# Kernel optimization log

Hardware: AMD Instinct MI355X
Metric: run time of the kernel (lower is better)

## Reference

```python
import jax, jax.numpy as jnp
import numpy as np

B, N, C, D, K, H, A = 4, 2048, 128, 128, 16, 64, 512


def _rn(k, shape, s):
    return (jax.random.normal(k, shape) * s).astype(jnp.float32)


def setup_inputs():
    ks = jax.random.split(jax.random.key(0), 40)
    w = lambda i, o, c: _rn(ks[i], (o, c), 0.02)
    b = lambda i, o: _rn(ks[i + 20], (o,), 0.02)
    p = {}
    p["xyz"] = _rn(ks[0], (B, 3, N), 1.0)
    p["pos"] = _rn(ks[1], (B, 2, N), 1.0)
    p["key"] = _rn(ks[2], (B, C, N), 1.0)
    p["query"] = _rn(ks[3], (B, C, N), 1.0)
    p["mv_w1"] = w(4, C, 2 * C); p["mv_b1"] = b(4, C)
    p["mv_w2"] = w(5, C, C);     p["mv_b2"] = b(5, C)
    p["mv_ws"] = w(6, C, 2 * C); p["mv_bs"] = b(6, C)
    p["wk"] = w(7, D, C); p["bk"] = b(7, D)
    p["wq"] = w(8, D, C); p["bq"] = b(8, D)
    p["wv"] = w(9, D, C); p["bv"] = b(9, D)
    p["xyz_w1"] = w(10, H, 3); p["xyz_b1"] = b(10, H)
    p["xyz_w2"] = w(11, D, H); p["xyz_b2"] = b(11, D)
    p["pos_w1"] = w(12, H, 2); p["pos_b1"] = b(12, H)
    p["pos_w2"] = w(13, D, H); p["pos_b2"] = b(13, D)
    p["xat_w1"] = w(14, A, D); p["xat_b1"] = b(14, A)
    p["xat_w2"] = w(15, D, A); p["xat_b2"] = b(15, D)
    p["at_w1"] = w(16, A, D); p["at_b1"] = b(16, A)
    p["at_w2"] = w(17, D, A); p["at_b2"] = b(17, D)
    p["wkq"] = w(18, C, D); p["bkq"] = b(18, C)
    p["wend"] = w(19, C, D); p["bend"] = b(19, C)
    return p


def c1(w, b, x):  # 1x1 Conv1d: (O,C) on (B,C,N)
    return jnp.einsum('oc,bcn->bon', w, x) + b[None, :, None]


def c2(w, b, x):  # 1x1 Conv2d: (O,C) on (B,C,N,K)
    return jnp.einsum('oc,bcnk->bonk', w, x) + b[None, :, None, None]


def mlp2(w1, b1, w2, b2, x):
    return c2(w2, b2, jax.nn.relu(c2(w1, b1, x)))


def softmax_one(x):  # exp(x-m) / (1 + sum exp(x-m)) over last axis
    m = jnp.max(x, axis=-1, keepdims=True)
    e = jnp.exp(x - m)
    return e / (1.0 + jnp.sum(e, axis=-1, keepdims=True))


def knn_idx(pts, k):  # pts: (B, N, d) -> (B, N, k) indices, include_self=True
    sq = jnp.sum(pts * pts, axis=-1)
    d2 = sq[:, :, None] + sq[:, None, :] - 2.0 * jnp.einsum('bnd,bmd->bnm', pts, pts)
    return jnp.argsort(d2, axis=-1)[:, :, :k]


def group(f, idx):  # f: (B,C,N), idx: (B,N,K) -> (B,C,N,K)
    return jax.vmap(lambda a, i: a[:, i])(f, idx)


def reference(xyz, pos, key, query, mv_w1, mv_b1, mv_w2, mv_b2, mv_ws, mv_bs,
              wk, bk, wq, bq, wv, bv, xyz_w1, xyz_b1, xyz_w2, xyz_b2,
              pos_w1, pos_b1, pos_w2, pos_b2, xat_w1, xat_b1, xat_w2, xat_b2,
              at_w1, at_b1, at_w2, at_b2, wkq, bkq, wend, bend):
    cat = jnp.concatenate([key, query], axis=1)  # (B, 2C, N)
    # MLP_Res
    value = c1(mv_w2, mv_b2, jax.nn.relu(c1(mv_w1, mv_b1, cat))) + c1(mv_ws, mv_bs, cat)
    identity = value
    k = c1(wk, bk, key)
    q = c1(wq, bq, query)
    v = c1(wv, bv, value)
    # ---- block 1: xyz-space kNN attention ----
    idx1 = knn_idx(jnp.swapaxes(xyz, 1, 2), K)           # (B,N,K)
    kq_rel = k[..., None] - group(q, idx1)               # (B,D,N,K)
    xyz_rel = xyz[..., None] - group(xyz, idx1)          # (B,3,N,K)
    xyz_emb = mlp2(xyz_w1, xyz_b1, xyz_w2, xyz_b2, xyz_rel)
    xa = softmax_one(mlp2(xat_w1, xat_b1, xat_w2, xat_b2, kq_rel + xyz_emb))
    agg = jnp.sum(xa * (v[..., None] + xyz_emb), axis=-1)  # (B,D,N)
    value = c1(wkq, bkq, agg) + identity
    value = c1(wv, bv, value)
    # ---- block 2: pos-space kNN attention ----
    idx2 = knn_idx(jnp.swapaxes(pos, 1, 2), K)
    qk_rel = q[..., None] - group(k, idx2)
    pos_rel = pos[..., None] - group(pos, idx2)
    pos_emb = mlp2(pos_w1, pos_b1, pos_w2, pos_b2, pos_rel)
    at = softmax_one(mlp2(at_w1, at_b1, at_w2, at_b2, qk_rel + pos_emb))
    agg = jnp.sum(at * (value[..., None] + pos_emb), axis=-1)
    y = c1(wend, bend, agg)
    return y + identity
```

## Files before the change

kernel.cpp:

```cpp
#include <hip/hip_runtime.h>
#include <hip/hip_bf16.h>

typedef __hip_bfloat16 bf16;
typedef unsigned long long ull;

#define BB 4
#define NN 2048
#define CCH 128
#define DDM 128
#define KNB 16
#define HHD 64
#define AAD 512
#define PP (BB*NN)

typedef __attribute__((ext_vector_type(8))) short short8;
typedef __attribute__((ext_vector_type(16))) float f32x16;

__device__ __forceinline__ float b2f(bf16 x) { return __bfloat162float(x); }
__device__ __forceinline__ bf16 f2b(float x) { return __float2bfloat16(x); }

__device__ __forceinline__ float ldany(const void* p, size_t i, int f32) {
  return f32 ? ((const float*)p)[i] : __bfloat162float(((const bf16*)p)[i]);
}

__device__ __forceinline__ long pack4(float a, float b, float c, float d) {
  union { bf16 h[4]; long l; } u;
  u.h[0] = f2b(a); u.h[1] = f2b(b); u.h[2] = f2b(c); u.h[3] = f2b(d);
  return u.l;
}
__device__ __forceinline__ void unpack4(long l, float* o) {
  union { bf16 h[4]; long l; } u; u.l = l;
  o[0] = b2f(u.h[0]); o[1] = b2f(u.h[1]); o[2] = b2f(u.h[2]); o[3] = b2f(u.h[3]);
}

__device__ __forceinline__ short8 ldfrag(const bf16* base, int row, int stride, int k0, int hl) {
  const bf16* p = base + (size_t)row * stride + k0 + (hl << 3);
  union { short8 v; long l[2]; } u;
  u.l[0] = *(const long*)p;
  u.l[1] = *(const long*)(p + 4);
  return u.v;
}

__device__ __forceinline__ f32x16 MFMA(short8 a, short8 b, f32x16 c) {
  return __builtin_amdgcn_mfma_f32_32x32x16_bf16(a, b, c, 0, 0, 0);
}

struct PtrArr { const void* p[36]; int n[36]; };
struct CvtTab { int src[16]; int off[16]; int n[16]; int isb[16]; };
struct G4 { const bf16* X[4]; int K[4]; int woff[4]; int boff[4]; bf16* out[4]; int relu[4]; };

__global__ __launch_bounds__(256) void sniff_kern(PtrArr pa, int* __restrict__ flags) {
  int t = blockIdx.x;
  const bf16* x = (const bf16*)pa.p[t];
  int n = pa.n[t]; if (n > 4096) n = 4096;
  __shared__ int cnt;
  if (threadIdx.x == 0) cnt = 0;
  __syncthreads();
  int c = 0;
  for (int i = threadIdx.x; i < n; i += 256) {
    float v = fabsf(__bfloat162float(x[i]));
    if (v == 0.f || (v >= 1e-6f && v <= 1024.f)) c++;
  }
  atomicAdd(&cnt, c);
  __syncthreads();
  if (threadIdx.x == 0) flags[t] = (cnt >= (n * 7) / 8) ? 0 : 1;
}

__global__ __launch_bounds__(256) void cvtprep_kern(PtrArr pa, CvtTab tab,
                                                    const int* __restrict__ flags,
                                                    bf16* __restrict__ warena, float* __restrict__ barena,
                                                    bf16* __restrict__ w1img0, bf16* __restrict__ w2img0,
                                                    bf16* __restrict__ cw2img0, float* __restrict__ fb0,
                                                    bf16* __restrict__ w1img1, bf16* __restrict__ w2img1,
                                                    bf16* __restrict__ cw2img1, float* __restrict__ fb1) {
  int y = blockIdx.y;
  if (y >= 2) {
    int e = y - 2;
    int i = blockIdx.x * 256 + threadIdx.x;
    if (i >= tab.n[e]) return;
    float v = ldany(pa.p[tab.src[e]], i, flags[tab.src[e]]);
    if (tab.isb[e]) barena[tab.off[e] + i] = v;
    else warena[tab.off[e] + i] = f2b(v);
    return;
  }
  int set = y;
  int cIdx = set ? 20 : 16, aIdx = set ? 28 : 24, dd = set ? 2 : 3;
  bf16* w1img = set ? w1img1 : w1img0;
  bf16* w2img = set ? w2img1 : w2img0;
  bf16* cw2img = set ? cw2img1 : cw2img0;
  float* fb = set ? fb1 : fb0;
  const void* cw1 = pa.p[cIdx];     const void* cb1 = pa.p[cIdx + 1];
  const void* cw2 = pa.p[cIdx + 2]; const void* cb2 = pa.p[cIdx + 3];
  const void* aw1 = pa.p[aIdx];     const void* ab1 = pa.p[aIdx + 1];
  const void* aw2 = pa.p[aIdx + 2]; const void* ab2 = pa.p[aIdx + 3];
  int i = blockIdx.x * 256 + threadIdx.x;
  const int fcw1 = flags[cIdx], fcb1 = flags[cIdx + 1];
  const int fcw2 = flags[cIdx + 2], fcb2 = flags[cIdx + 3];
  const int faw1 = flags[aIdx], fab1 = flags[aIdx + 1];
  const int faw2 = flags[aIdx + 2], fab2 = flags[aIdx + 3];
  float* ab1f = fb;
  float* ab2f = fb + 512;
  float* cb1f = fb + 640;
  float* cb2f = fb + 704;
  float* cw1f = fb + 832;
  if (i < 65536) {
    int hg = i >> 7, c = i & 127;
    w1img[(size_t)hg * 132 + c] = f2b(ldany(aw1, i, faw1));
  } else if (i < 131072) {
    int j = i - 65536;
    int o = j >> 9, hh = j & 511;
    int ac = hh >> 7, hloc = hh & 127;
    w2img[(size_t)(ac * 128 + o) * 132 + hloc] = f2b(ldany(aw2, j, faw2));
  } else if (i < 139264) {
    int j = i - 131072;
    int o = j >> 6, h = j & 63;
    cw2img[o * 68 + h] = f2b(ldany(cw2, j, fcw2));
  } else if (i < 139776) {
    int j = i - 139264; ab1f[j] = ldany(ab1, j, fab1);
  } else if (i < 139904) {
    int j = i - 139776; ab2f[j] = ldany(ab2, j, fab2);
  } else if (i < 139968) {
    int j = i - 139904; cb1f[j] = ldany(cb1, j, fcb1);
  } else if (i < 140096) {
    int j = i - 139968; cb2f[j] = ldany(cb2, j, fcb2);
  } else if (i < 140288) {
    int j = i - 140096;
    int h = j / 3, c = j % 3;
    cw1f[j] = (c < dd) ? ldany(cw1, h * dd + c, fcw1) : 0.f;
  }
}

__global__ __launch_bounds__(256) void trall_kern(const void* __restrict__ keyp,
                                                  const void* __restrict__ qryp,
                                                  const void* __restrict__ xyzp,
                                                  const void* __restrict__ posp,
                                                  const int* __restrict__ flags,
                                                  bf16* __restrict__ catT,
                                                  float* __restrict__ xyzT,
                                                  float* __restrict__ posT) {
  int bx = blockIdx.x;
  if (bx < 512) {
    __shared__ float tile[64][65];
    int xx = bx & 31, yy = (bx >> 5) & 1, zz = bx >> 6;
    int b = zz & 3, half = zz >> 2;
    const void* src = half ? qryp : keyp;
    const int f32 = flags[2 + half];
    int n0 = xx * 64, c0 = yy * 64;
    int tx = threadIdx.x & 63, ty = threadIdx.x >> 6;
    for (int r = ty; r < 64; r += 4)
      tile[r][tx] = ldany(src, (size_t)(b * 128 + c0 + r) * NN + n0 + tx, f32);
    __syncthreads();
    for (int r = ty; r < 64; r += 4)
      catT[(size_t)(b * NN + n0 + r) * 256 + half * 128 + c0 + tx] = __float2bfloat16(tile[tx][r]);
    return;
  }
  int cb = bx - 512;
  int which = cb >> 7;
  const void* src = which ? posp : xyzp;
  float* dst = which ? posT : xyzT;
  int dd = which ? 2 : 3;
  const int f32 = flags[which];
  int i = (cb & 127) * 256 * 2 + threadIdx.x;
  for (int rep = 0; rep < 2; ++rep, i += 256) {
    if (i < PP * 4) {
      int p = i >> 2, j = i & 3;
      int b = p >> 11, n = p & (NN - 1);
      dst[i] = (j < dd) ? ldany(src, (size_t)(b * dd + j) * NN + n, f32) : 0.f;
    }
  }
}

__global__ __launch_bounds__(512) void mega_kern(
    const float* __restrict__ xyzT, const float* __restrict__ posT,
    int* __restrict__ idx1, int* __restrict__ idx2,
    G4 g, const bf16* __restrict__ warena, const float* __restrict__ barena) {
  __shared__ __attribute__((aligned(16))) char smem[33280];
  int bx = blockIdx.x;
  int tid = threadIdx.x, lane = tid & 63, wvv = tid >> 6;
  if (bx < 2048) {
    float4* cds = (float4*)smem;
    int set = bx >> 10;
    int pblk = bx & 1023;
    const float* coordsT = set ? posT : xyzT;
    int* idxout = set ? idx2 : idx1;
    int p0 = pblk * 8, b = p0 >> 11;
    for (int j = tid; j < NN; j += 512)
      cds[j] = *(const float4*)&coordsT[((size_t)(b << 11) + j) * 4];
    __syncthreads();
    int p = p0 + wvv, n = p & (NN - 1);
    float4 cc = cds[n];
    float sqi = __fadd_rn(__fadd_rn(__fmul_rn(cc.x, cc.x), __fmul_rn(cc.y, cc.y)),
                          __fmul_rn(cc.z, cc.z));
    ull t[32];
#pragma unroll
    for (int s = 0; s < 32; ++s) {
      int j = (s << 6) | lane;
      float4 q = cds[j];
      float sqj = __fadd_rn(__fadd_rn(__fmul_rn(q.x, q.x), __fmul_rn(q.y, q.y)),
                            __fmul_rn(q.z, q.z));
      float dt  = __fadd_rn(__fadd_rn(__fmul_rn(cc.x, q.x), __fmul_rn(cc.y, q.y)),
                            __fmul_rn(cc.z, q.z));
      float d2 = __fsub_rn(__fadd_rn(sqi, sqj), __fmul_rn(2.f, dt));
      unsigned u = __float_as_uint(d2);
      u = (u & 0x80000000u) ? ~u : (u | 0x80000000u);
      t[s] = ((ull)u << 32) | (unsigned)j;
    }
#pragma unroll
    for (int k = 2; k <= 32; k <<= 1) {
#pragma unroll
      for (int j = k >> 1; j > 0; j >>= 1) {
#pragma unroll
        for (int i = 0; i < 32; ++i) {
          int l = i ^ j;
          if (l > i) {
            bool up = ((i & k) == 0);
            ull a = t[i], c = t[l];
            ull lo = a < c ? a : c;
            ull hi = a < c ? c : a;
            t[i] = up ? lo : hi;
            t[l] = up ? hi : lo;
          }
        }
      }
    }
    for (int r = 0; r < KNB; ++r) {
      ull h = t[0];
      ull m = h;
#pragma unroll
      for (int off = 1; off < 64; off <<= 1) {
        ull o = __shfl_xor(m, off);
        m = o < m ? o : m;
      }
      if (lane == 0) idxout[(size_t)p * KNB + r] = (int)(m & 0xffffffffu);
      if (h == m) {
#pragma unroll
        for (int i = 0; i < 15; ++i) t[i] = t[i + 1];
        t[15] = ~0ull;
      }
    }
    return;
  }
  {
    bf16* XT = (bf16*)smem;
    int bx2 = bx - 2048;
    int op = bx2 >> 7, ptile = bx2 & 127;
    const bf16* X = g.X[op];
    int K = g.K[op];
    const bf16* Wb = warena + g.woff[op];
    const float* bias = barena + g.boff[op];
    bf16* out = g.out[op];
    int relu = g.relu[op];
    int hl = lane >> 5, cA = lane & 31;
    int p0 = ptile * 64;
    int SK = K + 4;
    int kc = K >> 3;
    for (int c = tid; c < 64 * kc; c += 512) {
      int r = c / kc, col = (c % kc) << 3;
      *(float4*)&XT[r * SK + col] = *(const float4*)&X[(size_t)(p0 + r) * 256 + col];
    }
    __syncthreads();
    int o0 = (wvv & 3) * 32;
    int tt = wvv >> 2;
    f32x16 acc;
#pragma unroll
    for (int r = 0; r < 16; ++r) {
      int o = o0 + (r & 3) + 8 * (r >> 2) + 4 * hl;
      acc[r] = bias[o];
    }
    for (int ks = 0; ks < (K >> 4); ++ks) {
      short8 af = ldfrag(Wb, o0 + cA, K, ks * 16, hl);
      short8 b0 = ldfrag(XT, tt * 32 + cA, SK, ks * 16, hl);
      acc = MFMA(af, b0, acc);
    }
    int m = p0 + tt * 32 + cA;
#pragma unroll
    for (int q = 0; q < 4; ++q) {
      int ob = o0 + 8 * q + 4 * hl;
      float v[4] = {acc[4*q+0], acc[4*q+1], acc[4*q+2], acc[4*q+3]};
      if (relu) {
        v[0] = fmaxf(v[0], 0.f); v[1] = fmaxf(v[1], 0.f);
        v[2] = fmaxf(v[2], 0.f); v[3] = fmaxf(v[3], 0.f);
      }
      *(long*)(out + (size_t)m * 128 + ob) = pack4(v[0], v[1], v[2], v[3]);
    }
  }
}

__global__ __launch_bounds__(256) void gemm_chain_kern(
    const bf16* __restrict__ X, const bf16* __restrict__ warena,
    const float* __restrict__ barena,
    int w1off, int b1off, const bf16* __restrict__ add1, bf16* __restrict__ out1,
    int w2off, int b2off, bf16* __restrict__ out2) {
  __shared__ __attribute__((aligned(16))) bf16 XT[32 * 132];
  __shared__ __attribute__((aligned(16))) bf16 YT[32 * 132];
  int tid = threadIdx.x, lane = tid & 63, wv = tid >> 6;
  int hl = lane >> 5, cA = lane & 31;
  int p0 = blockIdx.x * 32;
  for (int c = tid; c < 32 * 16; c += 256) {
    int r = c >> 4, col = (c & 15) << 3;
    *(float4*)&XT[r * 132 + col] = *(const float4*)&X[(size_t)(p0 + r) * 128 + col];
  }
  __syncthreads();
  int o0 = wv * 32;
  const bf16* W1 = warena + w1off;
  const float* b1 = barena + b1off;
  f32x16 acc;
#pragma unroll
  for (int r = 0; r < 16; ++r) {
    int o = o0 + (r & 3) + 8 * (r >> 2) + 4 * hl;
    acc[r] = b1[o];
  }
#pragma unroll
  for (int ks = 0; ks < 8; ++ks) {
    short8 af = ldfrag(W1, o0 + cA, 128, ks * 16, hl);
    short8 b0 = ldfrag(XT, cA, 132, ks * 16, hl);
    acc = MFMA(af, b0, acc);
  }
  int m = p0 + cA;
#pragma unroll
  for (int q = 0; q < 4; ++q) {
    int ob = o0 + 8 * q + 4 * hl;
    float v[4] = {acc[4*q+0], acc[4*q+1], acc[4*q+2], acc[4*q+3]};
    if (add1) {
      float av[4];
      unpack4(*(const long*)(add1 + (size_t)m * 128 + ob), av);
      v[0] += av[0]; v[1] += av[1]; v[2] += av[2]; v[3] += av[3];
    }
    long pk = pack4(v[0], v[1], v[2], v[3]);
    *(long*)&YT[cA * 132 + ob] = pk;
    if (out1) *(long*)(out1 + (size_t)m * 128 + ob) = pk;
  }
  __syncthreads();
  const bf16* W2 = warena + w2off;
  const float* b2 = barena + b2off;
  f32x16 acc2;
#pragma unroll
  for (int r = 0; r < 16; ++r) {
    int o = o0 + (r & 3) + 8 * (r >> 2) + 4 * hl;
    acc2[r] = b2[o];
  }
#pragma unroll
  for (int ks = 0; ks < 8; ++ks) {
    short8 af = ldfrag(W2, o0 + cA, 128, ks * 16, hl);
    short8 b0 = ldfrag(YT, cA, 132, ks * 16, hl);
    acc2 = MFMA(af, b0, acc2);
  }
#pragma unroll
  for (int q = 0; q < 4; ++q) {
    int ob = o0 + 8 * q + 4 * hl;
    *(long*)(out2 + (size_t)m * 128 + ob) =
        pack4(acc2[4*q+0], acc2[4*q+1], acc2[4*q+2], acc2[4*q+3]);
  }
}

__global__ __launch_bounds__(256) void gemm32_kern(
    const bf16* __restrict__ X,
    const bf16* __restrict__ Wb, const float* __restrict__ bias,
    const bf16* __restrict__ add, bf16* __restrict__ out, int relu,
    void* __restrict__ outT, const int* __restrict__ flags) {
  __shared__ __attribute__((aligned(16))) bf16 XT[32 * 132];
  int tid = threadIdx.x, lane = tid & 63, wv = tid >> 6;
  int hl = lane >> 5, cA = lane & 31;
  int p0 = blockIdx.x * 32;
  for (int c = tid; c < 32 * 16; c += 256) {
    int r = c >> 4, col = (c & 15) << 3;
    *(float4*)&XT[r * 132 + col] = *(const float4*)&X[(size_t)(p0 + r) * 128 + col];
  }
  __syncthreads();
  int o0 = wv * 32;
  f32x16 acc;
#pragma unroll
  for (int r = 0; r < 16; ++r) {
    int o = o0 + (r & 3) + 8 * (r >> 2) + 4 * hl;
    acc[r] = bias[o];
  }
#pragma unroll
  for (int ks = 0; ks < 8; ++ks) {
    short8 af = ldfrag(Wb, o0 + cA, 128, ks * 16, hl);
    short8 b0 = ldfrag(XT, cA, 132, ks * 16, hl);
    acc = MFMA(af, b0, acc);
  }
  int m = p0 + cA;
  int f32o = outT ? flags[2] : 0;
  int b = m >> 11, n = m & (NN - 1);
#pragma unroll
  for (int q = 0; q < 4; ++q) {
    int ob = o0 + 8 * q + 4 * hl;
    float v[4] = {acc[4*q+0], acc[4*q+1], acc[4*q+2], acc[4*q+3]};
    if (add) {
      float av[4];
      unpack4(*(const long*)(add + (size_t)m * 128 + ob), av);
      v[0] += av[0]; v[1] += av[1]; v[2] += av[2]; v[3] += av[3];
    }
    if (relu) {
      v[0] = fmaxf(v[0], 0.f); v[1] = fmaxf(v[1], 0.f);
      v[2] = fmaxf(v[2], 0.f); v[3] = fmaxf(v[3], 0.f);
    }
    if (outT) {
#pragma unroll
      for (int i = 0; i < 4; ++i) {
        size_t oi = (size_t)(b * 128 + ob + i) * NN + n;
        if (f32o) ((float*)outT)[oi] = v[i];
        else ((bf16*)outT)[oi] = f2b(v[i]);
      }
    } else {
      *(long*)(out + (size_t)m * 128 + ob) = pack4(v[0], v[1], v[2], v[3]);
    }
  }
}

#define SMEM_BYTES 72192
__global__ __launch_bounds__(512, 4) void attn_mfma(
    const bf16* __restrict__ centerT, const bf16* __restrict__ gatherT,
    const float* __restrict__ coordsT, const bf16* __restrict__ vfeatT,
    const int* __restrict__ idx,
    const bf16* __restrict__ w1img, const bf16* __restrict__ w2img,
    const bf16* __restrict__ cw2img, const float* __restrict__ fb,
    bf16* __restrict__ aggT) {
  extern __shared__ char smem[];
  bf16* XS  = (bf16*)(smem);
  bf16* HT  = (bf16*)(smem + 33792);
  bf16* HC  = HT;
  bf16* CFE = (bf16*)(smem + 67584);
  bf16* VF  = (bf16*)(smem + 69632);
  int*  NID = (int*)(smem + 71680);
  const float* ab1f = fb;
  const float* ab2f = fb + 512;
  const float* cb1f = fb + 640;
  const float* cb2f = fb + 704;
  const float* cw1f = fb + 832;

  int tid = threadIdx.x, lane = tid & 63, wv = tid >> 6;
  int hl = lane >> 5, cA = lane & 31;
  int P0 = blockIdx.x * 8, b = P0 >> 11;

  if (tid < 128) NID[tid] = (b << 11) + idx[(size_t)(P0 + (tid >> 4)) * KNB + (tid & 15)];
  for (int i = tid; i < 1024; i += 512) {
    int g = i >> 7, d = i & 127;
    CFE[i] = centerT[(size_t)(P0 + g) * 128 + d];
    VF[i]  = vfeatT[(size_t)(P0 + g) * 128 + d];
  }
  __syncthreads();

  {
    int m = tid >> 2, sub = tid & 3;
    float4 ccd = *(const float4*)&coordsT[(size_t)(P0 + (m >> 4)) * 4];
    float4 nbd = *(const float4*)&coordsT[(size_t)NID[m] * 4];
    float r0 = ccd.x - nbd.x, r1 = ccd.y - nbd.y, r2 = ccd.z - nbd.z;
    int h0 = sub * 16;
    for (int hh = h0; hh < h0 + 16; hh += 4) {
      float a0 = fmaxf(cb1f[hh+0] + cw1f[(hh+0)*3]*r0 + cw1f[(hh+0)*3+1]*r1 + cw1f[(hh+0)*3+2]*r2, 0.f);
      float a1 = fmaxf(cb1f[hh+1] + cw1f[(hh+1)*3]*r0 + cw1f[(hh+1)*3+1]*r1 + cw1f[(hh+1)*3+2]*r2, 0.f);
      float a2 = fmaxf(cb1f[hh+2] + cw1f[(hh+2)*3]*r0 + cw1f[(hh+2)*3+1]*r1 + cw1f[(hh+2)*3+2]*r2, 0.f);
      float a3 = fmaxf(cb1f[hh+3] + cw1f[(hh+3)*3]*r0 + cw1f[(hh+3)*3+1]*r1 + cw1f[(hh+3)*3+2]*r2, 0.f);
      *(long*)&HC[m * 68 + hh] = pack4(a0, a1, a2, a3);
    }
    const bf16* grow = gatherT + (size_t)NID[m] * 128 + sub * 32;
    const bf16* crow = CFE + ((m >> 4) << 7) + sub * 32;
    for (int j = 0; j < 32; j += 4) {
      float gv[4], cv[4];
      unpack4(*(const long*)(grow + j), gv);
      unpack4(*(const long*)(crow + j), cv);
      *(long*)&XS[m * 132 + sub * 32 + j] =
          pack4(cv[0] - gv[0], cv[1] - gv[1], cv[2] - gv[2], cv[3] - gv[3]);
    }
  }
  __syncthreads();

  int r0s = (wv & 3) * 32;
  int mt0 = (wv >> 2) * 64;

  short8 pf[8];
#pragma unroll
  for (int ks = 0; ks < 8; ++ks)
    pf[ks] = ldfrag(w1img, r0s + cA, 132, ks * 16, hl);

  {
    f32x16 eacc[2];
#pragma unroll
    for (int r = 0; r < 16; ++r) {
      int o = r0s + (r & 3) + 8 * (r >> 2) + 4 * hl;
      float bv = cb2f[o];
      eacc[0][r] = bv; eacc[1][r] = bv;
    }
    for (int k0 = 0; k0 < 64; k0 += 16) {
      short8 af = ldfrag(cw2img, r0s + cA, 68, k0, hl);
      short8 b0 = ldfrag(HC, mt0 + cA, 68, k0, hl);
      short8 b1 = ldfrag(HC, mt0 + 32 + cA, 68, k0, hl);
      eacc[0] = MFMA(af, b0, eacc[0]);
      eacc[1] = MFMA(af, b1, eacc[1]);
    }
#pragma unroll
    for (int t = 0; t < 2; ++t) {
      int m = mt0 + t * 32 + cA;
#pragma unroll
      for (int q = 0; q < 4; ++q) {
        int ob = r0s + 8 * q + 4 * hl;
        bf16* px = &XS[m * 132 + ob];
        float xv[4];
        unpack4(*(long*)px, xv);
        *(long*)px = pack4(xv[0] + eacc[t][4*q+0], xv[1] + eacc[t][4*q+1],
                           xv[2] + eacc[t][4*q+2], xv[3] + eacc[t][4*q+3]);
      }
    }
  }
  __syncthreads();

  f32x16 acc2[2];
#pragma unroll
  for (int r = 0; r < 16; ++r) {
    int o = r0s + (r & 3) + 8 * (r >> 2) + 4 * hl;
    float bv = ab2f[o];
    acc2[0][r] = bv; acc2[1][r] = bv;
  }

  for (int ac = 0; ac < 4; ++ac) {
    const bf16* w2c = w2img + (size_t)ac * 16896;
    const bf16* w1n = w1img + (size_t)((ac + 1) & 3) * 16896;
    f32x16 acc1[2];
#pragma unroll
    for (int r = 0; r < 16; ++r) {
      int h = r0s + (r & 3) + 8 * (r >> 2) + 4 * hl;
      float bv = ab1f[ac * 128 + h];
      acc1[0][r] = bv; acc1[1][r] = bv;
    }
#pragma unroll
    for (int ks = 0; ks < 8; ++ks) {
      short8 af = pf[ks];
      short8 b0 = ldfrag(XS, mt0 + cA, 132, ks * 16, hl);
      short8 b1 = ldfrag(XS, mt0 + 32 + cA, 132, ks * 16, hl);
      pf[ks] = ldfrag(w2c, r0s + cA, 132, ks * 16, hl);
      acc1[0] = MFMA(af, b0, acc1[0]);
      acc1[1] = MFMA(af, b1, acc1[1]);
    }
    __syncthreads();
#pragma unroll
    for (int t = 0; t < 2; ++t) {
      int m = mt0 + t * 32 + cA;
#pragma unroll
      for (int q = 0; q < 4; ++q) {
        int hb = r0s + 8 * q + 4 * hl;
        *(long*)&HT[m * 132 + hb] =
            pack4(fmaxf(acc1[t][4*q+0], 0.f), fmaxf(acc1[t][4*q+1], 0.f),
                  fmaxf(acc1[t][4*q+2], 0.f), fmaxf(acc1[t][4*q+3], 0.f));
      }
    }
    __syncthreads();
#pragma unroll
    for (int ks = 0; ks < 8; ++ks) {
      short8 af = pf[ks];
      short8 b0 = ldfrag(HT, mt0 + cA, 132, ks * 16, hl);
      short8 b1 = ldfrag(HT, mt0 + 32 + cA, 132, ks * 16, hl);
      pf[ks] = ldfrag(w1n, r0s + cA, 132, ks * 16, hl);
      acc2[0] = MFMA(af, b0, acc2[0]);
      acc2[1] = MFMA(af, b1, acc2[1]);
    }
  }

  __syncthreads();
#pragma unroll
  for (int t = 0; t < 2; ++t) {
    int m = mt0 + t * 32 + cA;
#pragma unroll
    for (int q = 0; q < 4; ++q) {
      int ob = r0s + 8 * q + 4 * hl;
      *(long*)&HT[m * 132 + ob] = pack4(acc2[t][4*q+0], acc2[t][4*q+1],
                                        acc2[t][4*q+2], acc2[t][4*q+3]);
    }
  }
  __syncthreads();

  {
    int g = wv;
    int base = g * 16;
    float vbase0 = b2f(VF[g * 128 + lane])      - b2f(CFE[g * 128 + lane]);
    float vbase1 = b2f(VF[g * 128 + lane + 64]) - b2f(CFE[g * 128 + lane + 64]);
#pragma unroll
    for (int half = 0; half < 2; ++half) {
      int o = lane + half * 64;
      float vb = half ? vbase1 : vbase0;
      float e[16];
      float mx = -3.4e38f;
#pragma unroll
      for (int kk = 0; kk < 16; ++kk) {
        float x = b2f(HT[(base + kk) * 132 + o]);
        e[kk] = x;
        mx = fmaxf(mx, x);
      }
      float s = 0.f;
#pragma unroll
      for (int kk = 0; kk < 16; ++kk) { e[kk] = __expf(e[kk] - mx); s += e[kk]; }
      float inv = 1.f / (1.f + s);
      float acc = 0.f;
#pragma unroll
      for (int kk = 0; kk < 16; ++kk) {
        float xv = b2f(XS[(base + kk) * 132 + o]);
        float gv = b2f(gatherT[(size_t)NID[base + kk] * 128 + o]);
        acc += (e[kk] * inv) * (vb + xv + gv);
      }
      aggT[(size_t)(P0 + g) * 128 + o] = f2b(acc);
    }
  }
}

extern "C" void kernel_launch(void* const* d_in, const int* in_sizes, int n_in,
                              void* d_out, int out_size, void* d_ws, size_t ws_size,
                              hipStream_t stream) {
  int* flags = (int*)d_ws;
  bf16* catT = (bf16*)((float*)d_ws + 64);
  bf16* v0   = catT + (size_t)PP * 256;
  bf16* kT   = v0 + (size_t)PP * 128;
  bf16* qT   = kT + (size_t)PP * 128;
  bf16* sE   = qT + (size_t)PP * 128;
  bf16* sF   = sE + (size_t)PP * 128;
  bf16* sG   = sF + (size_t)PP * 128;
  float* xyzT = (float*)(sG + (size_t)PP * 128);
  float* posT = xyzT + (size_t)PP * 4;
  int* idx1 = (int*)(posT + (size_t)PP * 4);
  int* idx2 = idx1 + (size_t)PP * KNB;
  bf16* w1i1 = (bf16*)(idx2 + (size_t)PP * KNB);
  bf16* w2i1 = w1i1 + 67584;
  bf16* cw2i1 = w2i1 + 67584;
  bf16* w1i2 = cw2i1 + 8704;
  bf16* w2i2 = w1i2 + 67584;
  bf16* cw2i2 = w2i2 + 67584;
  float* fb1 = (float*)(cw2i2 + 8704);
  float* fb2 = fb1 + 1024;
  bf16* warena = (bf16*)(fb2 + 1024);
  float* barena = (float*)(warena + 163840);

  PtrArr pa;
  for (int i = 0; i < 36; ++i) { pa.p[i] = d_in[i]; pa.n[i] = in_sizes[i]; }
  sniff_kern<<<dim3(36), 256, 0, stream>>>(pa, flags);

  CvtTab tab;
  int wsrc[8] = {4, 8, 6, 10, 12, 14, 32, 34};
  int woff[8] = {0, 32768, 65536, 81920, 98304, 114688, 131072, 147456};
  int wn[8]   = {32768, 32768, 16384, 16384, 16384, 16384, 16384, 16384};
  int bsrc[8] = {5, 9, 7, 11, 13, 15, 33, 35};
  for (int e = 0; e < 8; ++e) {
    tab.src[e] = wsrc[e]; tab.off[e] = woff[e]; tab.n[e] = wn[e]; tab.isb[e] = 0;
    tab.src[8 + e] = bsrc[e]; tab.off[8 + e] = e * 128; tab.n[8 + e] = 128; tab.isb[8 + e] = 1;
  }
  cvtprep_kern<<<dim3(548, 18), 256, 0, stream>>>(pa, tab, flags, warena, barena,
                                                  w1i1, w2i1, cw2i1, fb1,
                                                  w1i2, w2i2, cw2i2, fb2);

  trall_kern<<<dim3(768), 256, 0, stream>>>(d_in[2], d_in[3], d_in[0], d_in[1],
                                            flags, catT, xyzT, posT);

  G4 g4;
  g4.X[0] = catT;       g4.K[0] = 256; g4.woff[0] = 0;      g4.boff[0] = 0;   g4.out[0] = sF; g4.relu[0] = 1;
  g4.X[1] = catT;       g4.K[1] = 256; g4.woff[1] = 32768;  g4.boff[1] = 128; g4.out[1] = sG; g4.relu[1] = 0;
  g4.X[2] = catT;       g4.K[2] = 128; g4.woff[2] = 81920;  g4.boff[2] = 384; g4.out[2] = kT; g4.relu[2] = 0;
  g4.X[3] = catT + 128; g4.K[3] = 128; g4.woff[3] = 98304;  g4.boff[3] = 512; g4.out[3] = qT; g4.relu[3] = 0;
  mega_kern<<<dim3(2048 + 512), 512, 0, stream>>>(xyzT, posT, idx1, idx2, g4, warena, barena);

  gemm_chain_kern<<<dim3(PP / 32), 256, 0, stream>>>(sF, warena, barena,
                                                     65536, 256, sG, v0,
                                                     114688, 640, sE);

  hipFuncSetAttribute((const void*)attn_mfma, hipFuncAttributeMaxDynamicSharedMemorySize, SMEM_BYTES);

  attn_mfma<<<dim3(PP / 8), 512, SMEM_BYTES, stream>>>(kT, qT, xyzT, sE, idx1,
                                                       w1i1, w2i1, cw2i1, fb1, sF);
  gemm_chain_kern<<<dim3(PP / 32), 256, 0, stream>>>(sF, warena, barena,
                                                     131072, 768, v0, nullptr,
                                                     114688, 640, sE);
  attn_mfma<<<dim3(PP / 8), 512, SMEM_BYTES, stream>>>(qT, kT, posT, sE, idx2,
                                                       w1i2, w2i2, cw2i2, fb2, sF);
  gemm32_kern<<<dim3(PP / 32), 256, 0, stream>>>(sF, warena + 147456, barena + 896, v0,
                                                 nullptr, 0, d_out, flags);
}
```

Before: 378.1 us.

## Fuse output projections into attention kernels and fold wv·wkq weights

Precomputes a combined weight wv·wkq and bias in an extra trall_kern block range, which lets the intermediate gemm_chain between the two attention blocks be dropped. Each attn_mfma now applies its output 1x1 projection plus residual directly from shared memory, so the separate gemm32 and gemm_chain launches and their aggT round-trips go away. It also caches the XS MFMA fragments in registers and replaces the full 32-element bitonic sort in kNN with two 16-element sorts plus a min-merge. The costs are more register pressure and an MFMA tile that only uses 8 of its 32 point columns in the fused epilogue. Folding the weights also changes rounding, since the combined product is stored in bf16.

```diff
diff --git a/kernel.cpp b/kernel.cpp
--- a/kernel.cpp
+++ b/kernel.cpp
@@ -137,8 +137,11 @@
                                                   const int* __restrict__ flags,
                                                   bf16* __restrict__ catT,
                                                   float* __restrict__ xyzT,
-                                                  float* __restrict__ posT) {
+                                                  float* __restrict__ posT,
+                                                  bf16* __restrict__ warena,
+                                                  float* __restrict__ barena) {
   int bx = blockIdx.x;
+  int tid = threadIdx.x;
   if (bx < 512) {
     __shared__ float tile[64][65];
     int xx = bx & 31, yy = (bx >> 5) & 1, zz = bx >> 6;
@@ -146,7 +149,7 @@
     const void* src = half ? qryp : keyp;
     const int f32 = flags[2 + half];
     int n0 = xx * 64, c0 = yy * 64;
-    int tx = threadIdx.x & 63, ty = threadIdx.x >> 6;
+    int tx = tid & 63, ty = tid >> 6;
     for (int r = ty; r < 64; r += 4)
       tile[r][tx] = ldany(src, (size_t)(b * 128 + c0 + r) * NN + n0 + tx, f32);
     __syncthreads();
@@ -154,19 +157,39 @@
       catT[(size_t)(b * NN + n0 + r) * 256 + half * 128 + c0 + tx] = __float2bfloat16(tile[tx][r]);
     return;
   }
-  int cb = bx - 512;
-  int which = cb >> 7;
-  const void* src = which ? posp : xyzp;
-  float* dst = which ? posT : xyzT;
-  int dd = which ? 2 : 3;
-  const int f32 = flags[which];
-  int i = (cb & 127) * 256 * 2 + threadIdx.x;
-  for (int rep = 0; rep < 2; ++rep, i += 256) {
-    if (i < PP * 4) {
-      int p = i >> 2, j = i & 3;
-      int b = p >> 11, n = p & (NN - 1);
-      dst[i] = (j < dd) ? ldany(src, (size_t)(b * dd + j) * NN + n, f32) : 0.f;
-    }
+  if (bx < 768) {
+    int cb = bx - 512;
+    int which = cb >> 7;
+    const void* src = which ? posp : xyzp;
+    float* dst = which ? posT : xyzT;
+    int dd = which ? 2 : 3;
+    const int f32 = flags[which];
+    int i = (cb & 127) * 256 * 2 + tid;
+    for (int rep = 0; rep < 2; ++rep, i += 256) {
+      if (i < PP * 4) {
+        int p = i >> 2, j = i & 3;
+        int b = p >> 11, n = p & (NN - 1);
+        dst[i] = (j < dd) ? ldany(src, (size_t)(b * dd + j) * NN + n, f32) : 0.f;
+      }
+    }
+    return;
+  }
+  int bx2 = bx - 768;
+  const bf16* wv = warena + 114688;
+  const bf16* wkq = warena + 131072;
+  if (bx2 < 64) {
+    int i = bx2 * 256 + tid;
+    int row = i >> 7, col = i & 127;
+    float acc = 0.f;
+    for (int k = 0; k < 128; ++k)
+      acc += b2f(wv[row * 128 + k]) * b2f(wkq[k * 128 + col]);
+    warena[163840 + i] = f2b(acc);
+  } else if (tid < 128) {
+    float acc = 0.f;
+    const float* bkq = barena + 768;
+    for (int k = 0; k < 128; ++k)
+      acc += b2f(wv[tid * 128 + k]) * bkq[k];
+    barena[1024 + tid] = acc;
   }
 }
 
@@ -206,20 +229,41 @@
       t[s] = ((ull)u << 32) | (unsigned)j;
     }
 #pragma unroll
-    for (int k = 2; k <= 32; k <<= 1) {
-#pragma unroll
-      for (int j = k >> 1; j > 0; j >>= 1) {
-#pragma unroll
-        for (int i = 0; i < 32; ++i) {
-          int l = i ^ j;
-          if (l > i) {
-            bool up = ((i & k) == 0);
-            ull a = t[i], c = t[l];
-            ull lo = a < c ? a : c;
-            ull hi = a < c ? c : a;
-            t[i] = up ? lo : hi;
-            t[l] = up ? hi : lo;
+    for (int base = 0; base < 32; base += 16) {
+#pragma unroll
+      for (int k = 2; k <= 16; k <<= 1) {
+#pragma unroll
+        for (int j = k >> 1; j > 0; j >>= 1) {
+#pragma unroll
+          for (int i = 0; i < 16; ++i) {
+            int l = i ^ j;
+            if (l > i) {
+              bool up = ((i & k) == 0);
+              ull a = t[base + i], c = t[base + l];
+              ull lo = a < c ? a : c;
+              ull hi = a < c ? c : a;
+              t[base + i] = up ? lo : hi;
+              t[base + l] = up ? hi : lo;
+            }
           }
+        }
+      }
+    }
+#pragma unroll
+    for (int i = 0; i < 16; ++i) {
+      ull a = t[i], c = t[31 - i];
+      t[i] = a < c ? a : c;
+    }
+#pragma unroll
+    for (int j = 8; j > 0; j >>= 1) {
+#pragma unroll
+      for (int i = 0; i < 16; ++i) {
+        int l = i ^ j;
+        if (l > i) {
+          ull a = t[i], c = t[l];
+          ull lo = a < c ? a : c;
+          ull hi = a < c ? c : a;
+          t[i] = lo; t[l] = hi;
         }
       }
     }
@@ -353,62 +397,6 @@
   }
 }
 
-__global__ __launch_bounds__(256) void gemm32_kern(
-    const bf16* __restrict__ X,
-    const bf16* __restrict__ Wb, const float* __restrict__ bias,
-    const bf16* __restrict__ add, bf16* __restrict__ out, int relu,
-    void* __restrict__ outT, const int* __restrict__ flags) {
-  __shared__ __attribute__((aligned(16))) bf16 XT[32 * 132];
-  int tid = threadIdx.x, lane = tid & 63, wv = tid >> 6;
-  int hl = lane >> 5, cA = lane & 31;
-  int p0 = blockIdx.x * 32;
-  for (int c = tid; c < 32 * 16; c += 256) {
-    int r = c >> 4, col = (c & 15) << 3;
-    *(float4*)&XT[r * 132 + col] = *(const float4*)&X[(size_t)(p0 + r) * 128 + col];
-  }
-  __syncthreads();
-  int o0 = wv * 32;
-  f32x16 acc;
-#pragma unroll
-  for (int r = 0; r < 16; ++r) {
-    int o = o0 + (r & 3) + 8 * (r >> 2) + 4 * hl;
-    acc[r] = bias[o];
-  }
-#pragma unroll
-  for (int ks = 0; ks < 8; ++ks) {
-    short8 af = ldfrag(Wb, o0 + cA, 128, ks * 16, hl);
-    short8 b0 = ldfrag(XT, cA, 132, ks * 16, hl);
-    acc = MFMA(af, b0, acc);
-  }
-  int m = p0 + cA;
-  int f32o = outT ? flags[2] : 0;
-  int b = m >> 11, n = m & (NN - 1);
-#pragma unroll
-  for (int q = 0; q < 4; ++q) {
-    int ob = o0 + 8 * q + 4 * hl;
-    float v[4] = {acc[4*q+0], acc[4*q+1], acc[4*q+2], acc[4*q+3]};
-    if (add) {
-      float av[4];
-      unpack4(*(const long*)(add + (size_t)m * 128 + ob), av);
-      v[0] += av[0]; v[1] += av[1]; v[2] += av[2]; v[3] += av[3];
-    }
-    if (relu) {
-      v[0] = fmaxf(v[0], 0.f); v[1] = fmaxf(v[1], 0.f);
-      v[2] = fmaxf(v[2], 0.f); v[3] = fmaxf(v[3], 0.f);
-    }
-    if (outT) {
-#pragma unroll
-      for (int i = 0; i < 4; ++i) {
-        size_t oi = (size_t)(b * 128 + ob + i) * NN + n;
-        if (f32o) ((float*)outT)[oi] = v[i];
-        else ((bf16*)outT)[oi] = f2b(v[i]);
-      }
-    } else {
-      *(long*)(out + (size_t)m * 128 + ob) = pack4(v[0], v[1], v[2], v[3]);
-    }
-  }
-}
-
 #define SMEM_BYTES 72192
 __global__ __launch_bounds__(512, 4) void attn_mfma(
     const bf16* __restrict__ centerT, const bf16* __restrict__ gatherT,
@@ -416,7 +404,9 @@
     const int* __restrict__ idx,
     const bf16* __restrict__ w1img, const bf16* __restrict__ w2img,
     const bf16* __restrict__ cw2img, const float* __restrict__ fb,
-    bf16* __restrict__ aggT) {
+    const bf16* __restrict__ wout, const float* __restrict__ bout,
+    const bf16* __restrict__ residG, void* __restrict__ outAny, int outMode,
+    const int* __restrict__ flags) {
   extern __shared__ char smem[];
   bf16* XS  = (bf16*)(smem);
   bf16* HT  = (bf16*)(smem + 33792);
@@ -506,6 +496,13 @@
   }
   __syncthreads();
 
+  short8 xsf[2][8];
+#pragma unroll
+  for (int ks = 0; ks < 8; ++ks) {
+    xsf[0][ks] = ldfrag(XS, mt0 + cA, 132, ks * 16, hl);
+    xsf[1][ks] = ldfrag(XS, mt0 + 32 + cA, 132, ks * 16, hl);
+  }
+
   f32x16 acc2[2];
 #pragma unroll
   for (int r = 0; r < 16; ++r) {
@@ -527,11 +524,9 @@
 #pragma unroll
     for (int ks = 0; ks < 8; ++ks) {
       short8 af = pf[ks];
-      short8 b0 = ldfrag(XS, mt0 + cA, 132, ks * 16, hl);
-      short8 b1 = ldfrag(XS, mt0 + 32 + cA, 132, ks * 16, hl);
       pf[ks] = ldfrag(w2c, r0s + cA, 132, ks * 16, hl);
-      acc1[0] = MFMA(af, b0, acc1[0]);
-      acc1[1] = MFMA(af, b1, acc1[1]);
+      acc1[0] = MFMA(af, xsf[0][ks], acc1[0]);
+      acc1[1] = MFMA(af, xsf[1][ks], acc1[1]);
     }
     __syncthreads();
 #pragma unroll
@@ -570,6 +565,7 @@
   }
   __syncthreads();
 
+  float agg0, agg1v;
   {
     int g = wv;
     int base = g * 16;
@@ -598,7 +594,58 @@
         float gv = b2f(gatherT[(size_t)NID[base + kk] * 128 + o]);
         acc += (e[kk] * inv) * (vb + xv + gv);
       }
-      aggT[(size_t)(P0 + g) * 128 + o] = f2b(acc);
+      if (half) agg1v = acc; else agg0 = acc;
+    }
+  }
+  __syncthreads();
+  {
+    int g = wv;
+    HT[g * 132 + lane] = f2b(agg0);
+    HT[g * 132 + lane + 64] = f2b(agg1v);
+  }
+  __syncthreads();
+
+  if (wv < 4) {
+    int o0m = wv * 32;
+    f32x16 acc;
+#pragma unroll
+    for (int r = 0; r < 16; ++r) {
+      int o = o0m + (r & 3) + 8 * (r >> 2) + 4 * hl;
+      acc[r] = bout[o];
+    }
+#pragma unroll
+    for (int ks = 0; ks < 8; ++ks) {
+      short8 af = ldfrag(wout, o0m + cA, 128, ks * 16, hl);
+      short8 b0 = ldfrag(HT, cA, 132, ks * 16, hl);
+      acc = MFMA(af, b0, acc);
+    }
+    int m = cA;
+    if (m < 8) {
+      int f32o = outMode ? flags[2] : 0;
+      int gp = P0 + m;
+      int gb = gp >> 11, gn = gp & (NN - 1);
+#pragma unroll
+      for (int q = 0; q < 4; ++q) {
+        int ob = o0m + 8 * q + 4 * hl;
+        float rv[4];
+        if (outMode) unpack4(*(const long*)(residG + (size_t)gp * 128 + ob), rv);
+        else         unpack4(*(long*)&VF[m * 128 + ob], rv);
+        float v0o = acc[4*q+0] + rv[0];
+        float v1o = acc[4*q+1] + rv[1];
+        float v2o = acc[4*q+2] + rv[2];
+        float v3o = acc[4*q+3] + rv[3];
+        if (outMode) {
+          float vv[4] = {v0o, v1o, v2o, v3o};
+#pragma unroll
+          for (int i = 0; i < 4; ++i) {
+            size_t oi = (size_t)(gb * 128 + ob + i) * NN + gn;
+            if (f32o) ((float*)outAny)[oi] = vv[i];
+            else ((bf16*)outAny)[oi] = f2b(vv[i]);
+          }
+        } else {
+          *(long*)((bf16*)outAny + (size_t)gp * 128 + ob) = pack4(v0o, v1o, v2o, v3o);
+        }
+      }
     }
   }
 }
@@ -627,7 +674,7 @@
   float* fb1 = (float*)(cw2i2 + 8704);
   float* fb2 = fb1 + 1024;
   bf16* warena = (bf16*)(fb2 + 1024);
-  float* barena = (float*)(warena + 163840);
+  float* barena = (float*)(warena + 180224);
 
   PtrArr pa;
   for (int i = 0; i < 36; ++i) { pa.p[i] = d_in[i]; pa.n[i] = in_sizes[i]; }
@@ -646,8 +693,8 @@
                                                   w1i1, w2i1, cw2i1, fb1,
                                                   w1i2, w2i2, cw2i2, fb2);
 
-  trall_kern<<<dim3(768), 256, 0, stream>>>(d_in[2], d_in[3], d_in[0], d_in[1],
-                                            flags, catT, xyzT, posT);
+  trall_kern<<<dim3(833), 256, 0, stream>>>(d_in[2], d_in[3], d_in[0], d_in[1],
+                                            flags, catT, xyzT, posT, warena, barena);
 
   G4 g4;
   g4.X[0] = catT;       g4.K[0] = 256; g4.woff[0] = 0;      g4.boff[0] = 0;   g4.out[0] = sF; g4.relu[0] = 1;
@@ -663,12 +710,11 @@
   hipFuncSetAttribute((const void*)attn_mfma, hipFuncAttributeMaxDynamicSharedMemorySize, SMEM_BYTES);
 
   attn_mfma<<<dim3(PP / 8), 512, SMEM_BYTES, stream>>>(kT, qT, xyzT, sE, idx1,
-                                                       w1i1, w2i1, cw2i1, fb1, sF);
-  gemm_chain_kern<<<dim3(PP / 32), 256, 0, stream>>>(sF, warena, barena,
-                                                     131072, 768, v0, nullptr,
-                                                     114688, 640, sE);
+                                                       w1i1, w2i1, cw2i1, fb1,
+                                                       warena + 163840, barena + 1024,
+                                                       nullptr, sE, 0, flags);
   attn_mfma<<<dim3(PP / 8), 512, SMEM_BYTES, stream>>>(qT, kT, posT, sE, idx2,
-                                                       w1i2, w2i2, cw2i2, fb2, sF);
-  gemm32_kern<<<dim3(PP / 32), 256, 0, stream>>>(sF, warena + 147456, barena + 896, v0,
-                                                 nullptr, 0, d_out, flags);
-}
+                                                       w1i2, w2i2, cw2i2, fb2,
+                                                       warena + 147456, barena + 896,
+                                                       v0, d_out, 1, flags);
+}
```

Result: slower. 496.7 us (+31.3%).
